# Performance work log

Hardware: AMD Instinct MI355X
Metric: run time of the kernel (lower is better)

Reference implementation:

```python
import jax, jax.numpy as jnp
import numpy as np

HALFKP = 64 * 5 * 64          # 20480
PAD = HALFKP                  # padding row index
L1, L2, L3 = 256, 31, 32
NB = 8                        # layer-stack / psqt buckets
EMB_DIM = L1 + NB             # 264


def setup_inputs() -> dict:
    key = jax.random.key(0)
    ks = jax.random.split(key, 16)
    B = 16384
    w_idx = jax.random.randint(ks[0], (B, 32), 0, HALFKP + 1)
    b_idx = jax.random.randint(ks[1], (B, 32), 0, HALFKP + 1)
    us = jax.random.uniform(ks[2], (B,), dtype=jnp.float32)
    them = jax.random.uniform(ks[3], (B,), dtype=jnp.float32)
    piece_count = jax.random.randint(ks[4], (B,), 2, 33)
    sigma = 0.025
    emb = jax.random.uniform(ks[5], (HALFKP + 1, EMB_DIM), jnp.float32, -sigma, sigma)
    emb = emb.at[PAD].set(0.0)
    def lin(k, out_f, in_f):
        bound = 1.0 / np.sqrt(in_f)
        k1, k2 = jax.random.split(k)
        W = jax.random.uniform(k1, (out_f, in_f), jnp.float32, -bound, bound)
        b = jax.random.uniform(k2, (out_f,), jnp.float32, -bound, bound)
        return W, b
    # StackedLinear init: replicate slot-0 weights across all buckets
    w1_0, b1_0 = lin(ks[6], L2 + 1, L1)
    w1 = jnp.tile(w1_0, (NB, 1)); b1 = jnp.tile(b1_0, NB)
    fw1 = jnp.zeros((L2 + 1, L1), jnp.float32)
    fb1 = jnp.zeros((L2 + 1,), jnp.float32)
    w2_0, b2_0 = lin(ks[7], L3, L2 * 2)
    w2 = jnp.tile(w2_0, (NB, 1)); b2 = jnp.tile(b2_0, NB)
    wo_0, _ = lin(ks[8], 1, L3)
    wo = jnp.tile(wo_0, (NB, 1)); bo = jnp.zeros((NB,), jnp.float32)
    return {"emb": emb, "w1": w1, "b1": b1, "fw1": fw1, "fb1": fb1,
            "w2": w2, "b2": b2, "wo": wo, "bo": bo,
            "us": us, "them": them,
            "w_idx": w_idx, "b_idx": b_idx, "piece_count": piece_count}


def reference(emb, w1, b1, fw1, fb1, w2, b2, wo, bo, us, them,
              w_idx, b_idx, piece_count):
    emb_eff = emb.at[PAD].set(0.0)                      # padding row contributes 0
    wp = emb_eff[w_idx].sum(axis=1)                     # [B, 264]
    bp = emb_eff[b_idx].sum(axis=1)
    w, wpsqt = wp[:, :L1], wp[:, L1:]
    b, bpsqt = bp[:, :L1], bp[:, L1:]
    us_c = us[:, None]; them_c = them[:, None]
    l0 = us_c * jnp.concatenate([w, b], 1) + them_c * jnp.concatenate([b, w], 1)
    l0 = jnp.clip(l0, 0.0, 1.0)                         # [B, 512]
    h = L1 // 2
    l0 = jnp.concatenate([l0[:, :h] * l0[:, h:2*h],
                          l0[:, 2*h:3*h] * l0[:, 3*h:]], 1) * (127.0 / 128.0)  # [B,256]
    bucket = jnp.clip((piece_count - 1) // 4, 0, 7)     # [B]
    # l1: factorized stacked linear, gather the bucket's slice only
    W1 = (w1 + jnp.tile(fw1, (NB, 1))).reshape(NB, L2 + 1, L1)
    B1 = (b1 + jnp.tile(fb1, NB)).reshape(NB, L2 + 1)
    l1c = jnp.einsum('bi,bji->bj', l0, W1[bucket]) + B1[bucket]   # [B,32]
    l1x, l1x_out = l1c[:, :L2], l1c[:, L2:]
    l1x = jnp.clip(jnp.concatenate([l1x * l1x * (255.0 / 256.0), l1x], 1), 0.0, 1.0)  # [B,62]
    W2 = w2.reshape(NB, L3, L2 * 2)
    l2x = jnp.clip(jnp.einsum('bi,bji->bj', l1x, W2[bucket]) + b2.reshape(NB, L3)[bucket], 0.0, 1.0)
    Wo = wo.reshape(NB, 1, L3)
    l3c = jnp.einsum('bi,bji->bj', l2x, Wo[bucket]) + bo.reshape(NB, 1)[bucket]       # [B,1]
    fc_out = l3c + l1x_out
    bk = bucket[:, None]
    psqt_out = (jnp.take_along_axis(wpsqt, bk, 1) - jnp.take_along_axis(bpsqt, bk, 1)) * (us_c - 0.5)
    return fc_out + psqt_out                            # [B,1]
```

## Files before the change

### kernel.cpp

```cpp
#include <hip/hip_runtime.h>

#define EMBD 264
#define NROWS 20481
#define QS 5080.0f
#define INVQS (1.0f/5080.0f)

typedef short short8 __attribute__((ext_vector_type(8)));
typedef float f32x4  __attribute__((ext_vector_type(4)));

__device__ __forceinline__ float clamp01(float x) { return fminf(fmaxf(x, 0.f), 1.f); }
__device__ __forceinline__ unsigned short f2bf(float f) {
    unsigned u = __float_as_uint(f);
    u += 0x7fffu + ((u >> 16) & 1u);
    return (unsigned short)(u >> 16);
}

__global__ void prep_emb8(const float* __restrict__ emb, unsigned int* __restrict__ emb8,
                          float* __restrict__ psqt) {
    const int r = blockIdx.x * 4 + (threadIdx.x >> 6);
    const int t = threadIdx.x & 63;
    if (r >= NROWS) return;
    const bool pad = (r == NROWS - 1);
    const float4 v = *((const float4*)(emb + (size_t)r * EMBD) + t);
    int q0 = pad ? 128 : (int)rintf(v.x * QS) + 128;
    int q1 = pad ? 128 : (int)rintf(v.y * QS) + 128;
    int q2 = pad ? 128 : (int)rintf(v.z * QS) + 128;
    int q3 = pad ? 128 : (int)rintf(v.w * QS) + 128;
    q0 = min(max(q0, 0), 255); q1 = min(max(q1, 0), 255);
    q2 = min(max(q2, 0), 255); q3 = min(max(q3, 0), 255);
    emb8[(size_t)r * 64 + t] = (unsigned)q0 | ((unsigned)q1 << 8) |
                               ((unsigned)q2 << 16) | ((unsigned)q3 << 24);
    if (t < 8) {
        float pv = emb[(size_t)r * EMBD + 256 + t];
        psqt[r * 8 + t] = pad ? 0.f : pv;
    }
}

__global__ void prep_tables(const float* __restrict__ w1, const float* __restrict__ fw1,
                            const float* __restrict__ b1, const float* __restrict__ fb1,
                            const float* __restrict__ w2,
                            unsigned short* __restrict__ w1b, float* __restrict__ b1c,
                            float* __restrict__ w2p) {
    const int e = blockIdx.x * 256 + threadIdx.x;
    const int bkt = e >> 13, rem = e & 8191;
    const int s = rem >> 10, rem2 = rem & 1023;
    const int nt = rem2 >> 9, rem3 = rem2 & 511;
    const int ln = rem3 >> 3, j = rem3 & 7;
    const int n  = nt * 16 + (ln & 15);
    const int hi = ln >> 4;
    const int k  = s * 32 + hi * 8 + j;
    const float v = w1[(bkt * 32 + n) * 256 + k] + fw1[n * 256 + k];
    w1b[e] = f2bf(v);
    if (e < 256) b1c[e] = b1[e] + fb1[e & 31];
    if (e < 16384) {
        const int jr = e >> 6, i = e & 63;
        float x = 0.f;
        if (i < 31) x = w2[jr * 62 + i];
        else if (i >= 32 && i < 63) x = w2[jr * 62 + i - 1];
        w2p[e] = x;
    }
}

__global__ __launch_bounds__(256) void nnue_fwd_mfma(
    const unsigned int* __restrict__ emb8,
    const float* __restrict__ psqt,
    const unsigned short* __restrict__ w1b,
    const float* __restrict__ b1c,
    const float* __restrict__ w2p,
    const float* __restrict__ b2,
    const float* __restrict__ wo,
    const float* __restrict__ bo,
    const float* __restrict__ us,
    const float* __restrict__ them,
    const int*   __restrict__ w_idx,
    const int*   __restrict__ b_idx,
    const int*   __restrict__ pcnt,
    float* __restrict__ out,
    int B)
{
    __shared__ unsigned short A_lds[16 * 280];
    __shared__ float l1c[8 * 16 * 36];
    __shared__ float psq_lds[16];
    __shared__ int   bkt_lds[16];

    const int tid  = threadIdx.x;
    const int lane = tid & 63;
    const int w    = tid >> 6;

    for (int rr = 0; rr < 4; ++rr) {
        const int m = w * 4 + rr;
        const int grow = __builtin_amdgcn_readfirstlane(blockIdx.x * 16 + m);

        const float usv = us[grow];
        const float thv = them[grow];
        int bucket = (pcnt[grow] - 1) >> 2;
        bucket = bucket > 7 ? 7 : bucket;
        bucket = __builtin_amdgcn_readfirstlane(bucket);

        const int* wrow = w_idx + grow * 32;
        const int* brow = b_idx + grow * 32;

        const int kk = lane & 31;
        const int pidx = (lane < 32) ? wrow[kk] : brow[kk];
        float ps = psqt[pidx * 8 + bucket];
        ps += __shfl_xor(ps, 16);
        ps += __shfl_xor(ps, 8);
        ps += __shfl_xor(ps, 4);
        ps += __shfl_xor(ps, 2);
        ps += __shfl_xor(ps, 1);
        const float psq_w = __shfl(ps, 0);
        const float psq_b = __shfl(ps, 32);

        unsigned aw0 = 0, aw1 = 0, ab0 = 0, ab1 = 0;
        const unsigned M = 0x00FF00FFu;
#pragma unroll
        for (int kb = 0; kb < 32; kb += 16) {
            unsigned vw[16], vb[16];
#pragma unroll
            for (int k2 = 0; k2 < 16; ++k2) {
                const int iw = __builtin_amdgcn_readfirstlane(wrow[kb + k2]);
                vw[k2] = emb8[(size_t)iw * 64 + lane];
            }
#pragma unroll
            for (int k2 = 0; k2 < 16; ++k2) {
                const int ib = __builtin_amdgcn_readfirstlane(brow[kb + k2]);
                vb[k2] = emb8[(size_t)ib * 64 + lane];
            }
#pragma unroll
            for (int k2 = 0; k2 < 16; ++k2) {
                aw0 += vw[k2] & M; aw1 += (vw[k2] >> 8) & M;
                ab0 += vb[k2] & M; ab1 += (vb[k2] >> 8) & M;
            }
        }
        float4 aw, ab;
        aw.x = ((int)(aw0 & 0xffffu) - 4096) * INVQS;
        aw.y = ((int)(aw1 & 0xffffu) - 4096) * INVQS;
        aw.z = ((int)(aw0 >> 16)     - 4096) * INVQS;
        aw.w = ((int)(aw1 >> 16)     - 4096) * INVQS;
        ab.x = ((int)(ab0 & 0xffffu) - 4096) * INVQS;
        ab.y = ((int)(ab1 & 0xffffu) - 4096) * INVQS;
        ab.z = ((int)(ab0 >> 16)     - 4096) * INVQS;
        ab.w = ((int)(ab1 >> 16)     - 4096) * INVQS;

        float4 p, q;
        p.x = clamp01(usv * aw.x + thv * ab.x);
        p.y = clamp01(usv * aw.y + thv * ab.y);
        p.z = clamp01(usv * aw.z + thv * ab.z);
        p.w = clamp01(usv * aw.w + thv * ab.w);
        q.x = clamp01(usv * ab.x + thv * aw.x);
        q.y = clamp01(usv * ab.y + thv * aw.y);
        q.z = clamp01(usv * ab.z + thv * aw.z);
        q.w = clamp01(usv * ab.w + thv * aw.w);

        float4 po, qo;
        po.x = __shfl_xor(p.x, 32); po.y = __shfl_xor(p.y, 32);
        po.z = __shfl_xor(p.z, 32); po.w = __shfl_xor(p.w, 32);
        qo.x = __shfl_xor(q.x, 32); qo.y = __shfl_xor(q.y, 32);
        qo.z = __shfl_xor(q.z, 32); qo.w = __shfl_xor(q.w, 32);
        const float c127 = 127.f / 128.f;
        float4 l0f;
        if (lane < 32) {
            l0f.x = p.x * po.x * c127; l0f.y = p.y * po.y * c127;
            l0f.z = p.z * po.z * c127; l0f.w = p.w * po.w * c127;
        } else {
            l0f.x = q.x * qo.x * c127; l0f.y = q.y * qo.y * c127;
            l0f.z = q.z * qo.z * c127; l0f.w = q.w * qo.w * c127;
        }

        const unsigned lo  = (unsigned)f2bf(l0f.x) | ((unsigned)f2bf(l0f.y) << 16);
        const unsigned hi2 = (unsigned)f2bf(l0f.z) | ((unsigned)f2bf(l0f.w) << 16);
        *((unsigned long long*)&A_lds[m * 280 + lane * 4]) =
            ((unsigned long long)hi2 << 32) | (unsigned long long)lo;
        if (lane == 0) {
            psq_lds[m] = (psq_w - psq_b) * (usv - 0.5f);
            bkt_lds[m] = bucket;
        }
    }
    __syncthreads();

    {
        const int col = lane & 15;
        const int hi  = lane >> 4;
        f32x4 acc[2][2];
#pragma unroll
        for (int bb = 0; bb < 2; ++bb)
#pragma unroll
            for (int nt = 0; nt < 2; ++nt)
                acc[bb][nt] = (f32x4){0.f, 0.f, 0.f, 0.f};

#pragma unroll
        for (int s = 0; s < 8; ++s) {
            const short8 a = *((const short8*)&A_lds[col * 280 + s * 32 + hi * 8]);
#pragma unroll
            for (int bb = 0; bb < 2; ++bb) {
                const int bkt = w * 2 + bb;
#pragma unroll
                for (int nt = 0; nt < 2; ++nt) {
                    const short8 bf = *((const short8*)&w1b[(((bkt * 8 + s) * 2 + nt) * 64 + lane) * 8]);
                    acc[bb][nt] = __builtin_amdgcn_mfma_f32_16x16x32_bf16(a, bf, acc[bb][nt], 0, 0, 0);
                }
            }
        }
#pragma unroll
        for (int bb = 0; bb < 2; ++bb) {
            const int bkt = w * 2 + bb;
#pragma unroll
            for (int nt = 0; nt < 2; ++nt) {
                const float bias = b1c[bkt * 32 + nt * 16 + col];
#pragma unroll
                for (int reg = 0; reg < 4; ++reg) {
                    const int mr = hi * 4 + reg;
                    l1c[(bkt * 16 + mr) * 36 + nt * 16 + col] = acc[bb][nt][reg] + bias;
                }
            }
        }
    }
    __syncthreads();

    {
        const int row = tid >> 4;
        const int jj  = tid & 15;
        const int bkt = bkt_lds[row];
        const float4* crow = (const float4*)&l1c[(bkt * 16 + row) * 36];
        float4 c4[8];
#pragma unroll
        for (int b5 = 0; b5 < 8; ++b5) c4[b5] = crow[b5];

        const float4* wr0 = (const float4*)&w2p[(bkt * 32 + jj) * 64];
        const float4* wr1 = (const float4*)&w2p[(bkt * 32 + jj + 16) * 64];
        float acc0 = 0.f, acc1 = 0.f;
        const float kq = 255.f / 256.f;
#pragma unroll
        for (int b5 = 0; b5 < 8; ++b5) {
            const float4 cv = c4[b5];
            float4 sq, ln;
            sq.x = clamp01(cv.x * cv.x * kq); ln.x = clamp01(cv.x);
            sq.y = clamp01(cv.y * cv.y * kq); ln.y = clamp01(cv.y);
            sq.z = clamp01(cv.z * cv.z * kq); ln.z = clamp01(cv.z);
            sq.w = clamp01(cv.w * cv.w * kq); ln.w = clamp01(cv.w);
            const float4 ws0 = wr0[b5], wl0 = wr0[8 + b5];
            const float4 ws1 = wr1[b5], wl1 = wr1[8 + b5];
            acc0 += sq.x * ws0.x + sq.y * ws0.y + sq.z * ws0.z + sq.w * ws0.w;
            acc0 += ln.x * wl0.x + ln.y * wl0.y + ln.z * wl0.z + ln.w * wl0.w;
            acc1 += sq.x * ws1.x + sq.y * ws1.y + sq.z * ws1.z + sq.w * ws1.w;
            acc1 += ln.x * wl1.x + ln.y * wl1.y + ln.z * wl1.z + ln.w * wl1.w;
        }
        const float t0 = clamp01(acc0 + b2[bkt * 32 + jj])      * wo[bkt * 32 + jj];
        const float t1 = clamp01(acc1 + b2[bkt * 32 + jj + 16]) * wo[bkt * 32 + jj + 16];
        float t = t0 + t1;
        t += __shfl_xor(t, 8);
        t += __shfl_xor(t, 4);
        t += __shfl_xor(t, 2);
        t += __shfl_xor(t, 1);
        if (jj == 0) {
            const int grow = blockIdx.x * 16 + row;
            if (grow < B)
                out[grow] = t + bo[bkt] + c4[7].w + psq_lds[row];
        }
    }
}

__global__ __launch_bounds__(256) void nnue_fwd_f32(
    const float* __restrict__ emb,
    const float* __restrict__ w1e, const float* __restrict__ fw1,
    const float* __restrict__ b1e, const float* __restrict__ fb1,
    const float* __restrict__ w2,  const float* __restrict__ b2,
    const float* __restrict__ wo,  const float* __restrict__ bo,
    const float* __restrict__ us,  const float* __restrict__ them,
    const int* __restrict__ w_idx, const int* __restrict__ b_idx,
    const int* __restrict__ pcnt,  float* __restrict__ out, int B)
{
    const int lane = threadIdx.x & 63;
    const int row  = blockIdx.x * 4 + (threadIdx.x >> 6);
    if (row >= B) return;
    const float usv = us[row];
    const float thv = them[row];
    int bucket = (pcnt[row] - 1) >> 2;
    bucket = bucket > 7 ? 7 : bucket;
    bucket = __builtin_amdgcn_readfirstlane(bucket);
    const int kk = lane & 31;
    const int myidx = (lane < 32) ? w_idx[row * 32 + kk] : b_idx[row * 32 + kk];
    float ps = emb[(size_t)myidx * EMBD + 256 + bucket];
    ps += __shfl_xor(ps, 16); ps += __shfl_xor(ps, 8);
    ps += __shfl_xor(ps, 4);  ps += __shfl_xor(ps, 2); ps += __shfl_xor(ps, 1);
    const float psq_w = __shfl(ps, 0);
    const float psq_b = __shfl(ps, 32);
    float4 aw = make_float4(0,0,0,0), ab = make_float4(0,0,0,0);
#pragma unroll
    for (int k = 0; k < 32; ++k) {
        const int iw = __shfl(myidx, k);
        const int ib = __shfl(myidx, 32 + k);
        const float4 vw = *((const float4*)(emb + (size_t)iw * EMBD) + lane);
        const float4 vb = *((const float4*)(emb + (size_t)ib * EMBD) + lane);
        aw.x += vw.x; aw.y += vw.y; aw.z += vw.z; aw.w += vw.w;
        ab.x += vb.x; ab.y += vb.y; ab.z += vb.z; ab.w += vb.w;
    }
    float4 p, q;
    p.x = clamp01(usv*aw.x + thv*ab.x); p.y = clamp01(usv*aw.y + thv*ab.y);
    p.z = clamp01(usv*aw.z + thv*ab.z); p.w = clamp01(usv*aw.w + thv*ab.w);
    q.x = clamp01(usv*ab.x + thv*aw.x); q.y = clamp01(usv*ab.y + thv*aw.y);
    q.z = clamp01(usv*ab.z + thv*aw.z); q.w = clamp01(usv*ab.w + thv*aw.w);
    float4 po, qo;
    po.x = __shfl_xor(p.x,32); po.y = __shfl_xor(p.y,32);
    po.z = __shfl_xor(p.z,32); po.w = __shfl_xor(p.w,32);
    qo.x = __shfl_xor(q.x,32); qo.y = __shfl_xor(q.y,32);
    qo.z = __shfl_xor(q.z,32); qo.w = __shfl_xor(q.w,32);
    const float c127 = 127.f/128.f;
    float4 l0f;
    if (lane < 32) { l0f.x=p.x*po.x*c127; l0f.y=p.y*po.y*c127; l0f.z=p.z*po.z*c127; l0f.w=p.w*po.w*c127; }
    else           { l0f.x=q.x*qo.x*c127; l0f.y=q.y*qo.y*c127; l0f.z=q.z*qo.z*c127; l0f.w=q.w*qo.w*c127; }
    float part[32];
    const float4* w1p = (const float4*)(w1e + (size_t)bucket * 8192);
    const float4* f1p = (const float4*)fw1;
#pragma unroll
    for (int j = 0; j < 32; ++j) {
        float4 wv = w1p[j*64 + lane];
        float4 fv = f1p[j*64 + lane];
        wv.x+=fv.x; wv.y+=fv.y; wv.z+=fv.z; wv.w+=fv.w;
        part[j] = l0f.x*wv.x + l0f.y*wv.y + l0f.z*wv.z + l0f.w*wv.w;
    }
#pragma unroll
    for (int j = 0; j < 32; ++j) {
        float v = part[j];
        v += __shfl_xor(v,32); v += __shfl_xor(v,16); v += __shfl_xor(v,8);
        v += __shfl_xor(v,4);  v += __shfl_xor(v,2);  v += __shfl_xor(v,1);
        part[j] = v + b1e[bucket*32 + j] + fb1[j];
    }
    const float l1x_out = part[31];
    float acc2 = 0.f;
    if (lane < 32) {
        const float* w2r = w2 + (size_t)(bucket*32 + lane) * 62;
#pragma unroll
        for (int i = 0; i < 31; ++i) {
            const float a = part[i];
            acc2 += clamp01(a*a*(255.f/256.f)) * w2r[i];
            acc2 += clamp01(a) * w2r[31+i];
        }
        acc2 += b2[bucket*32 + lane];
        acc2 = clamp01(acc2) * wo[bucket*32 + lane];
    }
    acc2 += __shfl_xor(acc2,16); acc2 += __shfl_xor(acc2,8);
    acc2 += __shfl_xor(acc2,4);  acc2 += __shfl_xor(acc2,2); acc2 += __shfl_xor(acc2,1);
    if (lane == 0)
        out[row] = acc2 + bo[bucket] + l1x_out + (psq_w - psq_b) * (usv - 0.5f);
}

extern "C" void kernel_launch(void* const* d_in, const int* in_sizes, int n_in,
                              void* d_out, int out_size, void* d_ws, size_t ws_size,
                              hipStream_t stream) {
    const float* emb  = (const float*)d_in[0];
    const float* w1   = (const float*)d_in[1];
    const float* b1   = (const float*)d_in[2];
    const float* fw1  = (const float*)d_in[3];
    const float* fb1  = (const float*)d_in[4];
    const float* w2   = (const float*)d_in[5];
    const float* b2   = (const float*)d_in[6];
    const float* wo   = (const float*)d_in[7];
    const float* bo   = (const float*)d_in[8];
    const float* us   = (const float*)d_in[9];
    const float* them = (const float*)d_in[10];
    const int*   wi   = (const int*)d_in[11];
    const int*   bi   = (const int*)d_in[12];
    const int*   pc   = (const int*)d_in[13];
    float* out = (float*)d_out;

    const int B = in_sizes[9];

    const size_t emb8_bytes = (size_t)NROWS * 256;
    const size_t psqt_bytes = (size_t)NROWS * 8 * 4;
    const size_t w1b_bytes  = 65536 * 2;
    const size_t b1c_bytes  = 256 * 4;
    const size_t w2p_bytes  = 16384 * 4;
    const size_t need = emb8_bytes + psqt_bytes + w1b_bytes + b1c_bytes + w2p_bytes;

    if (ws_size >= need && (B % 16) == 0) {
        char* p = (char*)d_ws;
        unsigned int*   emb8 = (unsigned int*)p;            p += emb8_bytes;
        float*          psqt = (float*)p;                   p += psqt_bytes;
        unsigned short* w1b  = (unsigned short*)p;          p += w1b_bytes;
        float*          b1c  = (float*)p;                   p += b1c_bytes;
        float*          w2p  = (float*)p;

        prep_emb8<<<(NROWS + 3) / 4, 256, 0, stream>>>(emb, emb8, psqt);
        prep_tables<<<256, 256, 0, stream>>>(w1, fw1, b1, fb1, w2, w1b, b1c, w2p);
        nnue_fwd_mfma<<<B / 16, 256, 0, stream>>>(emb8, psqt, w1b, b1c, w2p,
                                                  b2, wo, bo, us, them, wi, bi, pc, out, B);
    } else {
        nnue_fwd_f32<<<(B + 3) / 4, 256, 0, stream>>>(emb, w1, fw1, b1, fb1,
                                                      w2, b2, wo, bo, us, them, wi, bi, pc, out, B);
    }
}
```

Before: 139.2 us.

## Sort rows by bucket so each block runs MFMA only for its bucket range

Adds a per-block histogram kernel and a scatter kernel that build a permutation grouping batch rows by layer-stack bucket. The main kernel gathers rows through this permutation, and each wave skips the L1 MFMA work for buckets outside the block's min..max bucket range. Before, every block computed all 8 buckets for its 16 rows. This adds two small launches and indirect loads and scatter writes, and hardcodes B==16384 for the fast path.

```diff
diff --git a/kernel.cpp b/kernel.cpp
--- a/kernel.cpp
+++ b/kernel.cpp
@@ -61,6 +61,45 @@
     }
 }
 
+__global__ void bucket_hist(const int* __restrict__ pcnt, int* __restrict__ blkhist) {
+    __shared__ int h[8];
+    if (threadIdx.x < 8) h[threadIdx.x] = 0;
+    __syncthreads();
+    const int row = blockIdx.x * 256 + threadIdx.x;
+    int bkt = (pcnt[row] - 1) >> 2;
+    bkt = bkt > 7 ? 7 : bkt;
+    atomicAdd(&h[bkt], 1);
+    __syncthreads();
+    if (threadIdx.x < 8) blkhist[blockIdx.x * 8 + threadIdx.x] = h[threadIdx.x];
+}
+
+__global__ void bucket_scatter(const int* __restrict__ pcnt, const int* __restrict__ blkhist,
+                               int* __restrict__ order) {
+    __shared__ int lh[512];
+    __shared__ int lbase[8];
+    __shared__ int lcnt[8];
+    const int t = threadIdx.x, b = blockIdx.x;
+    for (int i = t; i < 512; i += 256) lh[i] = blkhist[i];
+    __syncthreads();
+    if (t < 8) {
+        int base = 0;
+        for (int j = 0; j < t; ++j) {
+            int s = 0;
+            for (int k = 0; k < 64; ++k) s += lh[k * 8 + j];
+            base += s;
+        }
+        for (int k = 0; k < b; ++k) base += lh[k * 8 + t];
+        lbase[t] = base;
+        lcnt[t] = 0;
+    }
+    __syncthreads();
+    const int row = b * 256 + t;
+    int bkt = (pcnt[row] - 1) >> 2;
+    bkt = bkt > 7 ? 7 : bkt;
+    const int r = atomicAdd(&lcnt[bkt], 1);
+    order[lbase[bkt] + r] = row;
+}
+
 __global__ __launch_bounds__(256) void nnue_fwd_mfma(
     const unsigned int* __restrict__ emb8,
     const float* __restrict__ psqt,
@@ -75,6 +114,7 @@
     const int*   __restrict__ w_idx,
     const int*   __restrict__ b_idx,
     const int*   __restrict__ pcnt,
+    const int*   __restrict__ order,
     float* __restrict__ out,
     int B)
 {
@@ -89,7 +129,7 @@
 
     for (int rr = 0; rr < 4; ++rr) {
         const int m = w * 4 + rr;
-        const int grow = __builtin_amdgcn_readfirstlane(blockIdx.x * 16 + m);
+        const int grow = __builtin_amdgcn_readfirstlane(order[blockIdx.x * 16 + m]);
 
         const float usv = us[grow];
         const float thv = them[grow];
@@ -179,38 +219,33 @@
     __syncthreads();
 
     {
+        const int bmin = __builtin_amdgcn_readfirstlane(bkt_lds[0]);
+        const int bmax = __builtin_amdgcn_readfirstlane(bkt_lds[15]);
         const int col = lane & 15;
         const int hi  = lane >> 4;
-        f32x4 acc[2][2];
-#pragma unroll
-        for (int bb = 0; bb < 2; ++bb)
-#pragma unroll
-            for (int nt = 0; nt < 2; ++nt)
-                acc[bb][nt] = (f32x4){0.f, 0.f, 0.f, 0.f};
-
-#pragma unroll
-        for (int s = 0; s < 8; ++s) {
-            const short8 a = *((const short8*)&A_lds[col * 280 + s * 32 + hi * 8]);
-#pragma unroll
-            for (int bb = 0; bb < 2; ++bb) {
-                const int bkt = w * 2 + bb;
+#pragma unroll
+        for (int bb = 0; bb < 2; ++bb) {
+            const int bkt = w * 2 + bb;
+            if (bkt < bmin || bkt > bmax) continue;
+            f32x4 acc[2];
+            acc[0] = (f32x4){0.f, 0.f, 0.f, 0.f};
+            acc[1] = (f32x4){0.f, 0.f, 0.f, 0.f};
+#pragma unroll
+            for (int s = 0; s < 8; ++s) {
+                const short8 a = *((const short8*)&A_lds[col * 280 + s * 32 + hi * 8]);
 #pragma unroll
                 for (int nt = 0; nt < 2; ++nt) {
                     const short8 bf = *((const short8*)&w1b[(((bkt * 8 + s) * 2 + nt) * 64 + lane) * 8]);
-                    acc[bb][nt] = __builtin_amdgcn_mfma_f32_16x16x32_bf16(a, bf, acc[bb][nt], 0, 0, 0);
+                    acc[nt] = __builtin_amdgcn_mfma_f32_16x16x32_bf16(a, bf, acc[nt], 0, 0, 0);
                 }
             }
-        }
-#pragma unroll
-        for (int bb = 0; bb < 2; ++bb) {
-            const int bkt = w * 2 + bb;
 #pragma unroll
             for (int nt = 0; nt < 2; ++nt) {
                 const float bias = b1c[bkt * 32 + nt * 16 + col];
 #pragma unroll
                 for (int reg = 0; reg < 4; ++reg) {
                     const int mr = hi * 4 + reg;
-                    l1c[(bkt * 16 + mr) * 36 + nt * 16 + col] = acc[bb][nt][reg] + bias;
+                    l1c[(bkt * 16 + mr) * 36 + nt * 16 + col] = acc[nt][reg] + bias;
                 }
             }
         }
@@ -253,9 +288,8 @@
         t += __shfl_xor(t, 2);
         t += __shfl_xor(t, 1);
         if (jj == 0) {
-            const int grow = blockIdx.x * 16 + row;
-            if (grow < B)
-                out[grow] = t + bo[bkt] + c4[7].w + psq_lds[row];
+            const int grow = order[blockIdx.x * 16 + row];
+            out[grow] = t + bo[bkt] + c4[7].w + psq_lds[row];
         }
     }
 }
@@ -366,25 +400,33 @@
 
     const int B = in_sizes[9];
 
-    const size_t emb8_bytes = (size_t)NROWS * 256;
-    const size_t psqt_bytes = (size_t)NROWS * 8 * 4;
-    const size_t w1b_bytes  = 65536 * 2;
-    const size_t b1c_bytes  = 256 * 4;
-    const size_t w2p_bytes  = 16384 * 4;
-    const size_t need = emb8_bytes + psqt_bytes + w1b_bytes + b1c_bytes + w2p_bytes;
-
-    if (ws_size >= need && (B % 16) == 0) {
+    const size_t emb8_bytes  = (size_t)NROWS * 256;
+    const size_t psqt_bytes  = (size_t)NROWS * 8 * 4;
+    const size_t w1b_bytes   = 65536 * 2;
+    const size_t b1c_bytes   = 256 * 4;
+    const size_t w2p_bytes   = 16384 * 4;
+    const size_t hist_bytes  = 64 * 8 * 4;
+    const size_t order_bytes = 16384 * 4;
+    const size_t need = emb8_bytes + psqt_bytes + w1b_bytes + b1c_bytes +
+                        w2p_bytes + hist_bytes + order_bytes;
+
+    if (ws_size >= need && B == 16384) {
         char* p = (char*)d_ws;
-        unsigned int*   emb8 = (unsigned int*)p;            p += emb8_bytes;
-        float*          psqt = (float*)p;                   p += psqt_bytes;
-        unsigned short* w1b  = (unsigned short*)p;          p += w1b_bytes;
-        float*          b1c  = (float*)p;                   p += b1c_bytes;
-        float*          w2p  = (float*)p;
+        unsigned int*   emb8    = (unsigned int*)p;     p += emb8_bytes;
+        float*          psqt    = (float*)p;            p += psqt_bytes;
+        unsigned short* w1b     = (unsigned short*)p;   p += w1b_bytes;
+        float*          b1c     = (float*)p;            p += b1c_bytes;
+        float*          w2p     = (float*)p;            p += w2p_bytes;
+        int*            blkhist = (int*)p;              p += hist_bytes;
+        int*            order   = (int*)p;
 
         prep_emb8<<<(NROWS + 3) / 4, 256, 0, stream>>>(emb, emb8, psqt);
         prep_tables<<<256, 256, 0, stream>>>(w1, fw1, b1, fb1, w2, w1b, b1c, w2p);
+        bucket_hist<<<64, 256, 0, stream>>>(pc, blkhist);
+        bucket_scatter<<<64, 256, 0, stream>>>(pc, blkhist, order);
         nnue_fwd_mfma<<<B / 16, 256, 0, stream>>>(emb8, psqt, w1b, b1c, w2p,
-                                                  b2, wo, bo, us, them, wi, bi, pc, out, B);
+                                                  b2, wo, bo, us, them, wi, bi, pc,
+                                                  order, out, B);
     } else {
         nnue_fwd_f32<<<(B + 3) / 4, 256, 0, stream>>>(emb, w1, fw1, b1, fb1,
                                                       w2, b2, wo, bo, us, them, wi, bi, pc, out, B);
```

New measurement: 141.5 us. Within noise of the previous version (+1.7%).

## Halve rows per block, merge prep kernels, and broadcast indices via readlane

Applied to the files above, without the earlier changes.

The two preprocessing kernels become one launch that branches on block index. The main kernel now handles 8 rows per block instead of 16, doubling the grid to raise occupancy and help hide the gather latency. Each wave loads its 64 feature indices with a single vector load and broadcasts them with readlane, replacing the repeated scalar index loads. In exchange, half of each 16-row MFMA tile and half of the stage-two threads now do unused work.

```diff
diff --git a/kernel.cpp b/kernel.cpp
--- a/kernel.cpp
+++ b/kernel.cpp
@@ -2,6 +2,7 @@
 
 #define EMBD 264
 #define NROWS 20481
+#define NR4   5121
 #define QS 5080.0f
 #define INVQS (1.0f/5080.0f)
 
@@ -15,49 +16,50 @@
     return (unsigned short)(u >> 16);
 }
 
-__global__ void prep_emb8(const float* __restrict__ emb, unsigned int* __restrict__ emb8,
-                          float* __restrict__ psqt) {
-    const int r = blockIdx.x * 4 + (threadIdx.x >> 6);
-    const int t = threadIdx.x & 63;
-    if (r >= NROWS) return;
-    const bool pad = (r == NROWS - 1);
-    const float4 v = *((const float4*)(emb + (size_t)r * EMBD) + t);
-    int q0 = pad ? 128 : (int)rintf(v.x * QS) + 128;
-    int q1 = pad ? 128 : (int)rintf(v.y * QS) + 128;
-    int q2 = pad ? 128 : (int)rintf(v.z * QS) + 128;
-    int q3 = pad ? 128 : (int)rintf(v.w * QS) + 128;
-    q0 = min(max(q0, 0), 255); q1 = min(max(q1, 0), 255);
-    q2 = min(max(q2, 0), 255); q3 = min(max(q3, 0), 255);
-    emb8[(size_t)r * 64 + t] = (unsigned)q0 | ((unsigned)q1 << 8) |
-                               ((unsigned)q2 << 16) | ((unsigned)q3 << 24);
-    if (t < 8) {
-        float pv = emb[(size_t)r * EMBD + 256 + t];
-        psqt[r * 8 + t] = pad ? 0.f : pv;
-    }
-}
-
-__global__ void prep_tables(const float* __restrict__ w1, const float* __restrict__ fw1,
-                            const float* __restrict__ b1, const float* __restrict__ fb1,
-                            const float* __restrict__ w2,
-                            unsigned short* __restrict__ w1b, float* __restrict__ b1c,
-                            float* __restrict__ w2p) {
-    const int e = blockIdx.x * 256 + threadIdx.x;
-    const int bkt = e >> 13, rem = e & 8191;
-    const int s = rem >> 10, rem2 = rem & 1023;
-    const int nt = rem2 >> 9, rem3 = rem2 & 511;
-    const int ln = rem3 >> 3, j = rem3 & 7;
-    const int n  = nt * 16 + (ln & 15);
-    const int hi = ln >> 4;
-    const int k  = s * 32 + hi * 8 + j;
-    const float v = w1[(bkt * 32 + n) * 256 + k] + fw1[n * 256 + k];
-    w1b[e] = f2bf(v);
-    if (e < 256) b1c[e] = b1[e] + fb1[e & 31];
-    if (e < 16384) {
-        const int jr = e >> 6, i = e & 63;
-        float x = 0.f;
-        if (i < 31) x = w2[jr * 62 + i];
-        else if (i >= 32 && i < 63) x = w2[jr * 62 + i - 1];
-        w2p[e] = x;
+__global__ void prep_all(const float* __restrict__ emb, unsigned int* __restrict__ emb8,
+                         float* __restrict__ psqt,
+                         const float* __restrict__ w1, const float* __restrict__ fw1,
+                         const float* __restrict__ b1, const float* __restrict__ fb1,
+                         const float* __restrict__ w2,
+                         unsigned short* __restrict__ w1b, float* __restrict__ b1c,
+                         float* __restrict__ w2p) {
+    if (blockIdx.x < NR4) {
+        const int r = blockIdx.x * 4 + (threadIdx.x >> 6);
+        const int t = threadIdx.x & 63;
+        if (r >= NROWS) return;
+        const bool pad = (r == NROWS - 1);
+        const float4 v = *((const float4*)(emb + (size_t)r * EMBD) + t);
+        int q0 = pad ? 128 : (int)rintf(v.x * QS) + 128;
+        int q1 = pad ? 128 : (int)rintf(v.y * QS) + 128;
+        int q2 = pad ? 128 : (int)rintf(v.z * QS) + 128;
+        int q3 = pad ? 128 : (int)rintf(v.w * QS) + 128;
+        q0 = min(max(q0, 0), 255); q1 = min(max(q1, 0), 255);
+        q2 = min(max(q2, 0), 255); q3 = min(max(q3, 0), 255);
+        emb8[(size_t)r * 64 + t] = (unsigned)q0 | ((unsigned)q1 << 8) |
+                                   ((unsigned)q2 << 16) | ((unsigned)q3 << 24);
+        if (t < 8) {
+            float pv = emb[(size_t)r * EMBD + 256 + t];
+            psqt[r * 8 + t] = pad ? 0.f : pv;
+        }
+    } else {
+        const int e = (blockIdx.x - NR4) * 256 + threadIdx.x;
+        const int bkt = e >> 13, rem = e & 8191;
+        const int s = rem >> 10, rem2 = rem & 1023;
+        const int nt = rem2 >> 9, rem3 = rem2 & 511;
+        const int ln = rem3 >> 3, j = rem3 & 7;
+        const int n  = nt * 16 + (ln & 15);
+        const int hi = ln >> 4;
+        const int k  = s * 32 + hi * 8 + j;
+        const float v = w1[(bkt * 32 + n) * 256 + k] + fw1[n * 256 + k];
+        w1b[e] = f2bf(v);
+        if (e < 256) b1c[e] = b1[e] + fb1[e & 31];
+        if (e < 16384) {
+            const int jr = e >> 6, i = e & 63;
+            float x = 0.f;
+            if (i < 31) x = w2[jr * 62 + i];
+            else if (i >= 32 && i < 63) x = w2[jr * 62 + i - 1];
+            w2p[e] = x;
+        }
     }
 }
 
@@ -79,17 +81,17 @@
     int B)
 {
     __shared__ unsigned short A_lds[16 * 280];
-    __shared__ float l1c[8 * 16 * 36];
-    __shared__ float psq_lds[16];
-    __shared__ int   bkt_lds[16];
+    __shared__ float l1c[8 * 8 * 36];
+    __shared__ float psq_lds[8];
+    __shared__ int   bkt_lds[8];
 
     const int tid  = threadIdx.x;
     const int lane = tid & 63;
     const int w    = tid >> 6;
 
-    for (int rr = 0; rr < 4; ++rr) {
-        const int m = w * 4 + rr;
-        const int grow = __builtin_amdgcn_readfirstlane(blockIdx.x * 16 + m);
+    for (int rr = 0; rr < 2; ++rr) {
+        const int m = w * 2 + rr;
+        const int grow = blockIdx.x * 8 + m;
 
         const float usv = us[grow];
         const float thv = them[grow];
@@ -97,12 +99,10 @@
         bucket = bucket > 7 ? 7 : bucket;
         bucket = __builtin_amdgcn_readfirstlane(bucket);
 
-        const int* wrow = w_idx + grow * 32;
-        const int* brow = b_idx + grow * 32;
-
         const int kk = lane & 31;
-        const int pidx = (lane < 32) ? wrow[kk] : brow[kk];
-        float ps = psqt[pidx * 8 + bucket];
+        const int idxv = (lane < 32) ? w_idx[grow * 32 + kk] : b_idx[grow * 32 + kk];
+
+        float ps = psqt[idxv * 8 + bucket];
         ps += __shfl_xor(ps, 16);
         ps += __shfl_xor(ps, 8);
         ps += __shfl_xor(ps, 4);
@@ -114,22 +114,17 @@
         unsigned aw0 = 0, aw1 = 0, ab0 = 0, ab1 = 0;
         const unsigned M = 0x00FF00FFu;
 #pragma unroll
-        for (int kb = 0; kb < 32; kb += 16) {
-            unsigned vw[16], vb[16];
+        for (int kb = 0; kb < 64; kb += 16) {
+            unsigned v[16];
 #pragma unroll
             for (int k2 = 0; k2 < 16; ++k2) {
-                const int iw = __builtin_amdgcn_readfirstlane(wrow[kb + k2]);
-                vw[k2] = emb8[(size_t)iw * 64 + lane];
+                const int idx = __builtin_amdgcn_readlane(idxv, kb + k2);
+                v[k2] = emb8[(size_t)idx * 64 + lane];
             }
 #pragma unroll
             for (int k2 = 0; k2 < 16; ++k2) {
-                const int ib = __builtin_amdgcn_readfirstlane(brow[kb + k2]);
-                vb[k2] = emb8[(size_t)ib * 64 + lane];
-            }
-#pragma unroll
-            for (int k2 = 0; k2 < 16; ++k2) {
-                aw0 += vw[k2] & M; aw1 += (vw[k2] >> 8) & M;
-                ab0 += vb[k2] & M; ab1 += (vb[k2] >> 8) & M;
+                if (kb + k2 < 32) { aw0 += v[k2] & M; aw1 += (v[k2] >> 8) & M; }
+                else              { ab0 += v[k2] & M; ab1 += (v[k2] >> 8) & M; }
             }
         }
         float4 aw, ab;
@@ -201,27 +196,29 @@
                 }
             }
         }
-#pragma unroll
-        for (int bb = 0; bb < 2; ++bb) {
-            const int bkt = w * 2 + bb;
-#pragma unroll
-            for (int nt = 0; nt < 2; ++nt) {
-                const float bias = b1c[bkt * 32 + nt * 16 + col];
-#pragma unroll
-                for (int reg = 0; reg < 4; ++reg) {
-                    const int mr = hi * 4 + reg;
-                    l1c[(bkt * 16 + mr) * 36 + nt * 16 + col] = acc[bb][nt][reg] + bias;
+        if (hi < 2) {
+#pragma unroll
+            for (int bb = 0; bb < 2; ++bb) {
+                const int bkt = w * 2 + bb;
+#pragma unroll
+                for (int nt = 0; nt < 2; ++nt) {
+                    const float bias = b1c[bkt * 32 + nt * 16 + col];
+#pragma unroll
+                    for (int reg = 0; reg < 4; ++reg) {
+                        const int mr = hi * 4 + reg;
+                        l1c[(bkt * 8 + mr) * 36 + nt * 16 + col] = acc[bb][nt][reg] + bias;
+                    }
                 }
             }
         }
     }
     __syncthreads();
 
-    {
+    if (tid < 128) {
         const int row = tid >> 4;
         const int jj  = tid & 15;
         const int bkt = bkt_lds[row];
-        const float4* crow = (const float4*)&l1c[(bkt * 16 + row) * 36];
+        const float4* crow = (const float4*)&l1c[(bkt * 8 + row) * 36];
         float4 c4[8];
 #pragma unroll
         for (int b5 = 0; b5 < 8; ++b5) c4[b5] = crow[b5];
@@ -253,9 +250,7 @@
         t += __shfl_xor(t, 2);
         t += __shfl_xor(t, 1);
         if (jj == 0) {
-            const int grow = blockIdx.x * 16 + row;
-            if (grow < B)
-                out[grow] = t + bo[bkt] + c4[7].w + psq_lds[row];
+            out[blockIdx.x * 8 + row] = t + bo[bkt] + c4[7].w + psq_lds[row];
         }
     }
 }
@@ -373,18 +368,18 @@
     const size_t w2p_bytes  = 16384 * 4;
     const size_t need = emb8_bytes + psqt_bytes + w1b_bytes + b1c_bytes + w2p_bytes;
 
-    if (ws_size >= need && (B % 16) == 0) {
+    if (ws_size >= need && (B % 8) == 0) {
         char* p = (char*)d_ws;
-        unsigned int*   emb8 = (unsigned int*)p;            p += emb8_bytes;
-        float*          psqt = (float*)p;                   p += psqt_bytes;
-        unsigned short* w1b  = (unsigned short*)p;          p += w1b_bytes;
-        float*          b1c  = (float*)p;                   p += b1c_bytes;
+        unsigned int*   emb8 = (unsigned int*)p;     p += emb8_bytes;
+        float*          psqt = (float*)p;            p += psqt_bytes;
+        unsigned short* w1b  = (unsigned short*)p;   p += w1b_bytes;
+        float*          b1c  = (float*)p;            p += b1c_bytes;
         float*          w2p  = (float*)p;
 
-        prep_emb8<<<(NROWS + 3) / 4, 256, 0, stream>>>(emb, emb8, psqt);
-        prep_tables<<<256, 256, 0, stream>>>(w1, fw1, b1, fb1, w2, w1b, b1c, w2p);
-        nnue_fwd_mfma<<<B / 16, 256, 0, stream>>>(emb8, psqt, w1b, b1c, w2p,
-                                                  b2, wo, bo, us, them, wi, bi, pc, out, B);
+        prep_all<<<NR4 + 256, 256, 0, stream>>>(emb, emb8, psqt,
+                                                w1, fw1, b1, fb1, w2, w1b, b1c, w2p);
+        nnue_fwd_mfma<<<B / 8, 256, 0, stream>>>(emb8, psqt, w1b, b1c, w2p,
+                                                 b2, wo, bo, us, them, wi, bi, pc, out, B);
     } else {
         nnue_fwd_f32<<<(B + 3) / 4, 256, 0, stream>>>(emb, w1, fw1, b1, fb1,
                                                       w2, b2, wo, bo, us, them, wi, bi, pc, out, B);
```

New measurement: 148.6 us. 1.07x slower.

## Split quantized embedding into half tables and gather two rows per load

Applied to the files above, without the earlier changes.

The 256-column int8 embedding table is split into two 128-byte half tables, so each wave load fetches two different feature rows (one per 32-lane half) instead of one full row. Partial sums from the two half-waves are combined with a cross-lane shuffle, and the l0 product pairs now line up inside a lane with no extra shuffles. The two prep kernels are merged into one launch to save launch overhead. In exchange, each wave issues twice as many per-row index reads and only half the lanes write to LDS, and the bounds check on the output store is removed.

```diff
diff --git a/kernel.cpp b/kernel.cpp
--- a/kernel.cpp
+++ b/kernel.cpp
@@ -2,6 +2,7 @@
 
 #define EMBD 264
 #define NROWS 20481
+#define NR4   5121
 #define QS 5080.0f
 #define INVQS (1.0f/5080.0f)
 
@@ -15,54 +16,59 @@
     return (unsigned short)(u >> 16);
 }
 
-__global__ void prep_emb8(const float* __restrict__ emb, unsigned int* __restrict__ emb8,
-                          float* __restrict__ psqt) {
-    const int r = blockIdx.x * 4 + (threadIdx.x >> 6);
-    const int t = threadIdx.x & 63;
-    if (r >= NROWS) return;
-    const bool pad = (r == NROWS - 1);
-    const float4 v = *((const float4*)(emb + (size_t)r * EMBD) + t);
-    int q0 = pad ? 128 : (int)rintf(v.x * QS) + 128;
-    int q1 = pad ? 128 : (int)rintf(v.y * QS) + 128;
-    int q2 = pad ? 128 : (int)rintf(v.z * QS) + 128;
-    int q3 = pad ? 128 : (int)rintf(v.w * QS) + 128;
-    q0 = min(max(q0, 0), 255); q1 = min(max(q1, 0), 255);
-    q2 = min(max(q2, 0), 255); q3 = min(max(q3, 0), 255);
-    emb8[(size_t)r * 64 + t] = (unsigned)q0 | ((unsigned)q1 << 8) |
-                               ((unsigned)q2 << 16) | ((unsigned)q3 << 24);
-    if (t < 8) {
-        float pv = emb[(size_t)r * EMBD + 256 + t];
-        psqt[r * 8 + t] = pad ? 0.f : pv;
+__global__ void prep_all(const float* __restrict__ emb,
+                         unsigned int* __restrict__ embA, unsigned int* __restrict__ embB,
+                         float* __restrict__ psqt,
+                         const float* __restrict__ w1, const float* __restrict__ fw1,
+                         const float* __restrict__ b1, const float* __restrict__ fb1,
+                         const float* __restrict__ w2,
+                         unsigned short* __restrict__ w1b, float* __restrict__ b1c,
+                         float* __restrict__ w2p) {
+    if (blockIdx.x < NR4) {
+        const int r = blockIdx.x * 4 + (threadIdx.x >> 6);
+        const int t = threadIdx.x & 63;
+        if (r >= NROWS) return;
+        const bool pad = (r == NROWS - 1);
+        const float4 v = *((const float4*)(emb + (size_t)r * EMBD) + t);
+        int q0 = pad ? 128 : (int)rintf(v.x * QS) + 128;
+        int q1 = pad ? 128 : (int)rintf(v.y * QS) + 128;
+        int q2 = pad ? 128 : (int)rintf(v.z * QS) + 128;
+        int q3 = pad ? 128 : (int)rintf(v.w * QS) + 128;
+        q0 = min(max(q0, 0), 255); q1 = min(max(q1, 0), 255);
+        q2 = min(max(q2, 0), 255); q3 = min(max(q3, 0), 255);
+        const unsigned packed = (unsigned)q0 | ((unsigned)q1 << 8) |
+                                ((unsigned)q2 << 16) | ((unsigned)q3 << 24);
+        if (t < 32) embA[(size_t)r * 32 + t] = packed;
+        else        embB[(size_t)r * 32 + (t - 32)] = packed;
+        if (t < 8) {
+            float pv = emb[(size_t)r * EMBD + 256 + t];
+            psqt[r * 8 + t] = pad ? 0.f : pv;
+        }
+    } else {
+        const int e = (blockIdx.x - NR4) * 256 + threadIdx.x;
+        const int bkt = e >> 13, rem = e & 8191;
+        const int s = rem >> 10, rem2 = rem & 1023;
+        const int nt = rem2 >> 9, rem3 = rem2 & 511;
+        const int ln = rem3 >> 3, j = rem3 & 7;
+        const int n  = nt * 16 + (ln & 15);
+        const int hi = ln >> 4;
+        const int k  = s * 32 + hi * 8 + j;
+        const float v = w1[(bkt * 32 + n) * 256 + k] + fw1[n * 256 + k];
+        w1b[e] = f2bf(v);
+        if (e < 256) b1c[e] = b1[e] + fb1[e & 31];
+        if (e < 16384) {
+            const int jr = e >> 6, i = e & 63;
+            float x = 0.f;
+            if (i < 31) x = w2[jr * 62 + i];
+            else if (i >= 32 && i < 63) x = w2[jr * 62 + i - 1];
+            w2p[e] = x;
+        }
     }
 }
 
-__global__ void prep_tables(const float* __restrict__ w1, const float* __restrict__ fw1,
-                            const float* __restrict__ b1, const float* __restrict__ fb1,
-                            const float* __restrict__ w2,
-                            unsigned short* __restrict__ w1b, float* __restrict__ b1c,
-                            float* __restrict__ w2p) {
-    const int e = blockIdx.x * 256 + threadIdx.x;
-    const int bkt = e >> 13, rem = e & 8191;
-    const int s = rem >> 10, rem2 = rem & 1023;
-    const int nt = rem2 >> 9, rem3 = rem2 & 511;
-    const int ln = rem3 >> 3, j = rem3 & 7;
-    const int n  = nt * 16 + (ln & 15);
-    const int hi = ln >> 4;
-    const int k  = s * 32 + hi * 8 + j;
-    const float v = w1[(bkt * 32 + n) * 256 + k] + fw1[n * 256 + k];
-    w1b[e] = f2bf(v);
-    if (e < 256) b1c[e] = b1[e] + fb1[e & 31];
-    if (e < 16384) {
-        const int jr = e >> 6, i = e & 63;
-        float x = 0.f;
-        if (i < 31) x = w2[jr * 62 + i];
-        else if (i >= 32 && i < 63) x = w2[jr * 62 + i - 1];
-        w2p[e] = x;
-    }
-}
-
 __global__ __launch_bounds__(256) void nnue_fwd_mfma(
-    const unsigned int* __restrict__ emb8,
+    const unsigned int* __restrict__ embA,
+    const unsigned int* __restrict__ embB,
     const float* __restrict__ psqt,
     const unsigned short* __restrict__ w1b,
     const float* __restrict__ b1c,
@@ -86,6 +92,7 @@
     const int tid  = threadIdx.x;
     const int lane = tid & 63;
     const int w    = tid >> 6;
+    const int g    = lane & 31;
 
     for (int rr = 0; rr < 4; ++rr) {
         const int m = w * 4 + rr;
@@ -100,8 +107,7 @@
         const int* wrow = w_idx + grow * 32;
         const int* brow = b_idx + grow * 32;
 
-        const int kk = lane & 31;
-        const int pidx = (lane < 32) ? wrow[kk] : brow[kk];
+        const int pidx = (lane < 32) ? wrow[g] : brow[g];
         float ps = psqt[pidx * 8 + bucket];
         ps += __shfl_xor(ps, 16);
         ps += __shfl_xor(ps, 8);
@@ -111,66 +117,77 @@
         const float psq_w = __shfl(ps, 0);
         const float psq_b = __shfl(ps, 32);
 
-        unsigned aw0 = 0, aw1 = 0, ab0 = 0, ab1 = 0;
-        const unsigned M = 0x00FF00FFu;
-#pragma unroll
-        for (int kb = 0; kb < 32; kb += 16) {
+        float4 wsum[2], bsum[2];
+#pragma unroll
+        for (int h = 0; h < 2; ++h) {
+            const unsigned int* T = h ? embB : embA;
             unsigned vw[16], vb[16];
 #pragma unroll
             for (int k2 = 0; k2 < 16; ++k2) {
-                const int iw = __builtin_amdgcn_readfirstlane(wrow[kb + k2]);
-                vw[k2] = emb8[(size_t)iw * 64 + lane];
+                const int i0 = __builtin_amdgcn_readfirstlane(wrow[2 * k2]);
+                const int i1 = __builtin_amdgcn_readfirstlane(wrow[2 * k2 + 1]);
+                const int base = (lane < 32) ? i0 : i1;
+                vw[k2] = T[(size_t)base * 32 + g];
             }
 #pragma unroll
             for (int k2 = 0; k2 < 16; ++k2) {
-                const int ib = __builtin_amdgcn_readfirstlane(brow[kb + k2]);
-                vb[k2] = emb8[(size_t)ib * 64 + lane];
+                const int i0 = __builtin_amdgcn_readfirstlane(brow[2 * k2]);
+                const int i1 = __builtin_amdgcn_readfirstlane(brow[2 * k2 + 1]);
+                const int base = (lane < 32) ? i0 : i1;
+                vb[k2] = T[(size_t)base * 32 + g];
             }
+            unsigned s0 = 0, s1 = 0, t0 = 0, t1 = 0;
+            const unsigned M = 0x00FF00FFu;
 #pragma unroll
             for (int k2 = 0; k2 < 16; ++k2) {
-                aw0 += vw[k2] & M; aw1 += (vw[k2] >> 8) & M;
-                ab0 += vb[k2] & M; ab1 += (vb[k2] >> 8) & M;
+                s0 += vw[k2] & M; s1 += (vw[k2] >> 8) & M;
+                t0 += vb[k2] & M; t1 += (vb[k2] >> 8) & M;
             }
-        }
-        float4 aw, ab;
-        aw.x = ((int)(aw0 & 0xffffu) - 4096) * INVQS;
-        aw.y = ((int)(aw1 & 0xffffu) - 4096) * INVQS;
-        aw.z = ((int)(aw0 >> 16)     - 4096) * INVQS;
-        aw.w = ((int)(aw1 >> 16)     - 4096) * INVQS;
-        ab.x = ((int)(ab0 & 0xffffu) - 4096) * INVQS;
-        ab.y = ((int)(ab1 & 0xffffu) - 4096) * INVQS;
-        ab.z = ((int)(ab0 >> 16)     - 4096) * INVQS;
-        ab.w = ((int)(ab1 >> 16)     - 4096) * INVQS;
-
-        float4 p, q;
-        p.x = clamp01(usv * aw.x + thv * ab.x);
-        p.y = clamp01(usv * aw.y + thv * ab.y);
-        p.z = clamp01(usv * aw.z + thv * ab.z);
-        p.w = clamp01(usv * aw.w + thv * ab.w);
-        q.x = clamp01(usv * ab.x + thv * aw.x);
-        q.y = clamp01(usv * ab.y + thv * aw.y);
-        q.z = clamp01(usv * ab.z + thv * aw.z);
-        q.w = clamp01(usv * ab.w + thv * aw.w);
-
-        float4 po, qo;
-        po.x = __shfl_xor(p.x, 32); po.y = __shfl_xor(p.y, 32);
-        po.z = __shfl_xor(p.z, 32); po.w = __shfl_xor(p.w, 32);
-        qo.x = __shfl_xor(q.x, 32); qo.y = __shfl_xor(q.y, 32);
-        qo.z = __shfl_xor(q.z, 32); qo.w = __shfl_xor(q.w, 32);
+            s0 += __shfl_xor(s0, 32); s1 += __shfl_xor(s1, 32);
+            t0 += __shfl_xor(t0, 32); t1 += __shfl_xor(t1, 32);
+            wsum[h].x = ((int)(s0 & 0xffffu) - 4096) * INVQS;
+            wsum[h].y = ((int)(s1 & 0xffffu) - 4096) * INVQS;
+            wsum[h].z = ((int)(s0 >> 16)     - 4096) * INVQS;
+            wsum[h].w = ((int)(s1 >> 16)     - 4096) * INVQS;
+            bsum[h].x = ((int)(t0 & 0xffffu) - 4096) * INVQS;
+            bsum[h].y = ((int)(t1 & 0xffffu) - 4096) * INVQS;
+            bsum[h].z = ((int)(t0 >> 16)     - 4096) * INVQS;
+            bsum[h].w = ((int)(t1 >> 16)     - 4096) * INVQS;
+        }
+
+        float4 plo, phi, qlo, qhi;
+        plo.x = clamp01(usv * wsum[0].x + thv * bsum[0].x);
+        plo.y = clamp01(usv * wsum[0].y + thv * bsum[0].y);
+        plo.z = clamp01(usv * wsum[0].z + thv * bsum[0].z);
+        plo.w = clamp01(usv * wsum[0].w + thv * bsum[0].w);
+        phi.x = clamp01(usv * wsum[1].x + thv * bsum[1].x);
+        phi.y = clamp01(usv * wsum[1].y + thv * bsum[1].y);
+        phi.z = clamp01(usv * wsum[1].z + thv * bsum[1].z);
+        phi.w = clamp01(usv * wsum[1].w + thv * bsum[1].w);
+        qlo.x = clamp01(usv * bsum[0].x + thv * wsum[0].x);
+        qlo.y = clamp01(usv * bsum[0].y + thv * wsum[0].y);
+        qlo.z = clamp01(usv * bsum[0].z + thv * wsum[0].z);
+        qlo.w = clamp01(usv * bsum[0].w + thv * wsum[0].w);
+        qhi.x = clamp01(usv * bsum[1].x + thv * wsum[1].x);
+        qhi.y = clamp01(usv * bsum[1].y + thv * wsum[1].y);
+        qhi.z = clamp01(usv * bsum[1].z + thv * wsum[1].z);
+        qhi.w = clamp01(usv * bsum[1].w + thv * wsum[1].w);
         const float c127 = 127.f / 128.f;
-        float4 l0f;
+
         if (lane < 32) {
-            l0f.x = p.x * po.x * c127; l0f.y = p.y * po.y * c127;
-            l0f.z = p.z * po.z * c127; l0f.w = p.w * po.w * c127;
-        } else {
-            l0f.x = q.x * qo.x * c127; l0f.y = q.y * qo.y * c127;
-            l0f.z = q.z * qo.z * c127; l0f.w = q.w * qo.w * c127;
-        }
-
-        const unsigned lo  = (unsigned)f2bf(l0f.x) | ((unsigned)f2bf(l0f.y) << 16);
-        const unsigned hi2 = (unsigned)f2bf(l0f.z) | ((unsigned)f2bf(l0f.w) << 16);
-        *((unsigned long long*)&A_lds[m * 280 + lane * 4]) =
-            ((unsigned long long)hi2 << 32) | (unsigned long long)lo;
+            const unsigned aLo = (unsigned)f2bf(plo.x * phi.x * c127) |
+                                 ((unsigned)f2bf(plo.y * phi.y * c127) << 16);
+            const unsigned aHi = (unsigned)f2bf(plo.z * phi.z * c127) |
+                                 ((unsigned)f2bf(plo.w * phi.w * c127) << 16);
+            *((unsigned long long*)&A_lds[m * 280 + g * 4]) =
+                ((unsigned long long)aHi << 32) | (unsigned long long)aLo;
+            const unsigned bLo = (unsigned)f2bf(qlo.x * qhi.x * c127) |
+                                 ((unsigned)f2bf(qlo.y * qhi.y * c127) << 16);
+            const unsigned bHi = (unsigned)f2bf(qlo.z * qhi.z * c127) |
+                                 ((unsigned)f2bf(qlo.w * qhi.w * c127) << 16);
+            *((unsigned long long*)&A_lds[m * 280 + 128 + g * 4]) =
+                ((unsigned long long)bHi << 32) | (unsigned long long)bLo;
+        }
         if (lane == 0) {
             psq_lds[m] = (psq_w - psq_b) * (usv - 0.5f);
             bkt_lds[m] = bucket;
@@ -253,9 +270,7 @@
         t += __shfl_xor(t, 2);
         t += __shfl_xor(t, 1);
         if (jj == 0) {
-            const int grow = blockIdx.x * 16 + row;
-            if (grow < B)
-                out[grow] = t + bo[bkt] + c4[7].w + psq_lds[row];
+            out[blockIdx.x * 16 + row] = t + bo[bkt] + c4[7].w + psq_lds[row];
         }
     }
 }
@@ -366,24 +381,25 @@
 
     const int B = in_sizes[9];
 
-    const size_t emb8_bytes = (size_t)NROWS * 256;
+    const size_t half_bytes = (size_t)NROWS * 128;
     const size_t psqt_bytes = (size_t)NROWS * 8 * 4;
     const size_t w1b_bytes  = 65536 * 2;
     const size_t b1c_bytes  = 256 * 4;
     const size_t w2p_bytes  = 16384 * 4;
-    const size_t need = emb8_bytes + psqt_bytes + w1b_bytes + b1c_bytes + w2p_bytes;
+    const size_t need = 2 * half_bytes + psqt_bytes + w1b_bytes + b1c_bytes + w2p_bytes;
 
     if (ws_size >= need && (B % 16) == 0) {
         char* p = (char*)d_ws;
-        unsigned int*   emb8 = (unsigned int*)p;            p += emb8_bytes;
-        float*          psqt = (float*)p;                   p += psqt_bytes;
-        unsigned short* w1b  = (unsigned short*)p;          p += w1b_bytes;
-        float*          b1c  = (float*)p;                   p += b1c_bytes;
+        unsigned int*   embA = (unsigned int*)p;     p += half_bytes;
+        unsigned int*   embB = (unsigned int*)p;     p += half_bytes;
+        float*          psqt = (float*)p;            p += psqt_bytes;
+        unsigned short* w1b  = (unsigned short*)p;   p += w1b_bytes;
+        float*          b1c  = (float*)p;            p += b1c_bytes;
         float*          w2p  = (float*)p;
 
-        prep_emb8<<<(NROWS + 3) / 4, 256, 0, stream>>>(emb, emb8, psqt);
-        prep_tables<<<256, 256, 0, stream>>>(w1, fw1, b1, fb1, w2, w1b, b1c, w2p);
-        nnue_fwd_mfma<<<B / 16, 256, 0, stream>>>(emb8, psqt, w1b, b1c, w2p,
+        prep_all<<<NR4 + 256, 256, 0, stream>>>(emb, embA, embB, psqt,
+                                                w1, fw1, b1, fb1, w2, w1b, b1c, w2p);
+        nnue_fwd_mfma<<<B / 16, 256, 0, stream>>>(embA, embB, psqt, w1b, b1c, w2p,
                                                   b2, wo, bo, us, them, wi, bi, pc, out, B);
     } else {
         nnue_fwd_f32<<<(B + 3) / 4, 256, 0, stream>>>(emb, w1, fw1, b1, fb1,
```

Measured after the change: 137.2 us. Within noise of the previous version (-1.5%).
